# Kernel optimization log

Hardware: AMD Instinct MI355X
Metric: run time of the kernel (lower is better)

The kernel has to match this reference:

```python
import jax, jax.numpy as jnp
import numpy as np

CUTOFF = 5.0
BOX_L = 60.0  # positions are scaled into a 60 A cube


def setup_inputs() -> dict:
    key = jax.random.key(0)
    N = 4096
    xyz = jax.random.uniform(key, (N, 3), dtype=jnp.float32) * BOX_L
    return {"xyz": xyz}


def reference(xyz):
    # All unordered pairs i<j (exclude_ii=True, no periodic box)
    N = xyz.shape[0]
    ii, jj = jnp.triu_indices(N, k=1)            # [P], P = N*(N-1)/2
    deltas = xyz[ii] - xyz[jj]                    # [P, 3]
    dist = jnp.sqrt(jnp.sum(deltas * deltas, axis=-1))  # [P]
    mask = dist < CUTOFF                          # within-cutoff pairs

    # jit-friendly equivalent of the torch NaN-mask compaction:
    # invalid pairs get index -1, zero delta/distance; n_pairs counts valid.
    pair_i = jnp.where(mask, ii, -1).astype(jnp.int32)
    pair_j = jnp.where(mask, jj, -1).astype(jnp.int32)
    pair_diff = jnp.where(mask[:, None], deltas, 0.0)
    pair_dist = jnp.where(mask, dist, 0.0)
    n_pairs = jnp.sum(mask).astype(jnp.int32).reshape(1)
    return pair_i, pair_j, pair_diff, pair_dist, n_pairs
```

## Files before the change

### kernel.cpp

```cpp
#include <hip/hip_runtime.h>


#define NSLOTS 1024

__global__ void zero_ws(int* __restrict__ ws) {
    int t = blockIdx.x * blockDim.x + threadIdx.x;
    if (t < NSLOTS) ws[t] = 0;
}

__global__ __launch_bounds__(256) void nl_kernel(const float* __restrict__ xyz,
                                                 float* __restrict__ out,
                                                 int* __restrict__ ws,
                                                 int N, int P) {
    const int i = blockIdx.y;
    const int jb = blockIdx.x * 256;
    if (jb + 255 <= i) return;
    const int j = jb + threadIdx.x;

    __shared__ int wcnt[4];

    bool valid = false;
    if (j > i) {
        const float xi = xyz[3 * i + 0];
        const float yi = xyz[3 * i + 1];
        const float zi = xyz[3 * i + 2];
        const float xj = xyz[3 * j + 0];
        const float yj = xyz[3 * j + 1];
        const float zj = xyz[3 * j + 2];
        const float dx = xi - xj;
        const float dy = yi - yj;
        const float dz = zi - zj;
        const float d2 = dx * dx + dy * dy + dz * dz;
        const float dist = sqrtf(d2);
        valid = dist < 5.0f;

        const int p = i * (N - 1) - (i * (i - 1)) / 2 + (j - i - 1);
        out[p]     = valid ? (float)i : -1.f;
        out[P + p] = valid ? (float)j : -1.f;
        const int q = 2 * P + 3 * p;
        out[q + 0] = valid ? dx : 0.f;
        out[q + 1] = valid ? dy : 0.f;
        out[q + 2] = valid ? dz : 0.f;
        out[5 * P + p] = valid ? dist : 0.f;
    }

    unsigned long long b = __ballot(valid);
    if ((threadIdx.x & 63) == 0) wcnt[threadIdx.x >> 6] = __popcll(b);
    __syncthreads();
    if (threadIdx.x == 0) {
        int c = wcnt[0] + wcnt[1] + wcnt[2] + wcnt[3];
        if (c) atomicAdd(&ws[(blockIdx.y * gridDim.x + blockIdx.x) & (NSLOTS - 1)], c);
    }
}

__global__ void finalize_kernel(float* __restrict__ out, const int* __restrict__ ws,
                                int pos) {
    const int t = threadIdx.x;
    int s = ws[t] + ws[t + 256] + ws[t + 512] + ws[t + 768];
    for (int o = 32; o > 0; o >>= 1) s += __shfl_down(s, o, 64);
    __shared__ int sh[4];
    if ((t & 63) == 0) sh[t >> 6] = s;
    __syncthreads();
    if (t == 0) out[pos] = (float)(sh[0] + sh[1] + sh[2] + sh[3]);
}

extern "C" void kernel_launch(void* const* d_in, const int* in_sizes, int n_in,
                              void* d_out, int out_size, void* d_ws, size_t ws_size,
                              hipStream_t stream) {
    const float* xyz = (const float*)d_in[0];
    float* out = (float*)d_out;
    int* ws = (int*)d_ws;

    const int N = in_sizes[0] / 3;
    const long long Pll = (long long)N * (N - 1) / 2;
    const int P = (int)Pll;

    zero_ws<<<4, 256, 0, stream>>>(ws);

    dim3 grid((N + 255) / 256, N - 1);
    nl_kernel<<<grid, 256, 0, stream>>>(xyz, out, ws, N, P);

    finalize_kernel<<<1, 256, 0, stream>>>(out, ws, 6 * P);
}
```

Baseline: 50.22 us.

## Linearize pair index with 4 pairs per thread and vectorized float4 stores

Replaces the 2D (row, column-block) grid with a 1D grid over the flat triangular pair index. Each thread recovers its row via a sqrt inversion and handles four consecutive pairs, writing each output section with 16-byte vector stores, including the interleaved xyz delta block. Per-block counts are written straight into per-block slots, which removes the workspace zeroing kernel and the atomics when there is enough workspace. The cost is a double-precision sqrt and small correction loops per thread. The vector stores also assume that P and the output offsets keep 16-byte alignment.

New measurement: 45.42 us. -9.6%, faster.

```diff
diff --git a/kernel.cpp b/kernel.cpp
--- a/kernel.cpp
+++ b/kernel.cpp
@@ -1,62 +1,86 @@
 #include <hip/hip_runtime.h>
 
 
-#define NSLOTS 1024
+typedef float f4 __attribute__((ext_vector_type(4)));
 
-__global__ void zero_ws(int* __restrict__ ws) {
+__global__ void zero_ws(int* __restrict__ ws, int n) {
     int t = blockIdx.x * blockDim.x + threadIdx.x;
-    if (t < NSLOTS) ws[t] = 0;
+    if (t < n) ws[t] = 0;
 }
 
 __global__ __launch_bounds__(256) void nl_kernel(const float* __restrict__ xyz,
                                                  float* __restrict__ out,
                                                  int* __restrict__ ws,
-                                                 int N, int P) {
-    const int i = blockIdx.y;
-    const int jb = blockIdx.x * 256;
-    if (jb + 255 <= i) return;
-    const int j = jb + threadIdx.x;
+                                                 int N, int P, int slots) {
+    const int p0 = (blockIdx.x * 256 + threadIdx.x) * 4;
+    int cnt = 0;
+    if (p0 < P) {
+        const double twoNm1 = (double)(2 * N - 1);
+        int i = (int)((twoNm1 - sqrt(twoNm1 * twoNm1 - 8.0 * (double)p0)) * 0.5);
+        if (i > N - 2) i = N - 2;
+        if (i < 0) i = 0;
+        int rs = i * (2 * N - 1 - i) / 2;
+        while (p0 < rs) { --i; rs -= (N - 1 - i); }
+        int next = rs + (N - 1 - i);
+        while (p0 >= next && i < N - 2) { ++i; rs = next; next += (N - 1 - i); }
 
-    __shared__ int wcnt[4];
+        float iv[4], jv[4], dxs[4], dys[4], dzs[4], dv[4];
+        #pragma unroll
+        for (int e = 0; e < 4; ++e) {
+            const int p = p0 + e;
+            while (p >= next && i < N - 2) { ++i; rs = next; next += (N - 1 - i); }
+            const int j = i + 1 + (p - rs);
+            float dx = 0.f, dy = 0.f, dz = 0.f, dist = 0.f, fi = -1.f, fj = -1.f;
+            if (p < P) {
+                const float ax = xyz[3 * i], ay = xyz[3 * i + 1], az = xyz[3 * i + 2];
+                const float bx = xyz[3 * j], by = xyz[3 * j + 1], bz = xyz[3 * j + 2];
+                const float tx = ax - bx, ty = ay - by, tz = az - bz;
+                const float d = sqrtf(tx * tx + ty * ty + tz * tz);
+                if (d < 5.0f) {
+                    fi = (float)i; fj = (float)j;
+                    dx = tx; dy = ty; dz = tz; dist = d;
+                    ++cnt;
+                }
+            }
+            iv[e] = fi; jv[e] = fj; dxs[e] = dx; dys[e] = dy; dzs[e] = dz; dv[e] = dist;
+        }
 
-    bool valid = false;
-    if (j > i) {
-        const float xi = xyz[3 * i + 0];
-        const float yi = xyz[3 * i + 1];
-        const float zi = xyz[3 * i + 2];
-        const float xj = xyz[3 * j + 0];
-        const float yj = xyz[3 * j + 1];
-        const float zj = xyz[3 * j + 2];
-        const float dx = xi - xj;
-        const float dy = yi - yj;
-        const float dz = zi - zj;
-        const float d2 = dx * dx + dy * dy + dz * dz;
-        const float dist = sqrtf(d2);
-        valid = dist < 5.0f;
-
-        const int p = i * (N - 1) - (i * (i - 1)) / 2 + (j - i - 1);
-        out[p]     = valid ? (float)i : -1.f;
-        out[P + p] = valid ? (float)j : -1.f;
-        const int q = 2 * P + 3 * p;
-        out[q + 0] = valid ? dx : 0.f;
-        out[q + 1] = valid ? dy : 0.f;
-        out[q + 2] = valid ? dz : 0.f;
-        out[5 * P + p] = valid ? dist : 0.f;
+        if (p0 + 4 <= P) {
+            *(f4*)(out + p0)     = (f4){iv[0], iv[1], iv[2], iv[3]};
+            *(f4*)(out + P + p0) = (f4){jv[0], jv[1], jv[2], jv[3]};
+            f4* dp = (f4*)(out + 2 * P + 3 * p0);
+            dp[0] = (f4){dxs[0], dys[0], dzs[0], dxs[1]};
+            dp[1] = (f4){dys[1], dzs[1], dxs[2], dys[2]};
+            dp[2] = (f4){dzs[2], dxs[3], dys[3], dzs[3]};
+            *(f4*)(out + 5 * P + p0) = (f4){dv[0], dv[1], dv[2], dv[3]};
+        } else {
+            for (int e = 0; e < 4 && p0 + e < P; ++e) {
+                const int p = p0 + e;
+                out[p] = iv[e]; out[P + p] = jv[e];
+                out[2 * P + 3 * p]     = dxs[e];
+                out[2 * P + 3 * p + 1] = dys[e];
+                out[2 * P + 3 * p + 2] = dzs[e];
+                out[5 * P + p] = dv[e];
+            }
+        }
     }
 
-    unsigned long long b = __ballot(valid);
-    if ((threadIdx.x & 63) == 0) wcnt[threadIdx.x >> 6] = __popcll(b);
+    for (int o = 32; o > 0; o >>= 1) cnt += __shfl_down(cnt, o, 64);
+    __shared__ int sh[4];
+    if ((threadIdx.x & 63) == 0) sh[threadIdx.x >> 6] = cnt;
     __syncthreads();
     if (threadIdx.x == 0) {
-        int c = wcnt[0] + wcnt[1] + wcnt[2] + wcnt[3];
-        if (c) atomicAdd(&ws[(blockIdx.y * gridDim.x + blockIdx.x) & (NSLOTS - 1)], c);
+        const int c = sh[0] + sh[1] + sh[2] + sh[3];
+        if ((int)gridDim.x <= slots) ws[blockIdx.x] = c;
+        else if (c) atomicAdd(&ws[blockIdx.x % slots], c);
     }
 }
 
 __global__ void finalize_kernel(float* __restrict__ out, const int* __restrict__ ws,
-                                int pos) {
+                                int n, int pos) {
     const int t = threadIdx.x;
-    int s = ws[t] + ws[t + 256] + ws[t + 512] + ws[t + 768];
+    int s = 0;
+    for (int k = t; k < n; k += 256) s += ws[k];
     for (int o = 32; o > 0; o >>= 1) s += __shfl_down(s, o, 64);
     __shared__ int sh[4];
     if ((t & 63) == 0) sh[t >> 6] = s;
@@ -72,13 +96,13 @@
     int* ws = (int*)d_ws;
 
     const int N = in_sizes[0] / 3;
-    const long long Pll = (long long)N * (N - 1) / 2;
-    const int P = (int)Pll;
+    const int P = (int)((long long)N * (N - 1) / 2);
 
-    zero_ws<<<4, 256, 0, stream>>>(ws);
+    const int nb = (P + 1023) / 1024;
+    const int cap = (int)(ws_size / 4);
+    const int slots = (nb <= cap) ? nb : (cap < 1 ? 1 : (cap > 1024 ? 1024 : cap));
+    if (nb > slots) zero_ws<<<(slots + 255) / 256, 256, 0, stream>>>(ws, slots);
 
-    dim3 grid((N + 255) / 256, N - 1);
-    nl_kernel<<<grid, 256, 0, stream>>>(xyz, out, ws, N, P);
-
-    finalize_kernel<<<1, 256, 0, stream>>>(out, ws, 6 * P);
+    nl_kernel<<<nb, 256, 0, stream>>>(xyz, out, ws, N, P, slots);
+    finalize_kernel<<<1, 256, 0, stream>>>(out, ws, slots, 6 * P);
 }
```
